# Performance work log

Measured on AMD Instinct MI355X. Metric: run time of the kernel, lower is better.

The kernel has to match this reference:

```python
import jax, jax.numpy as jnp
import numpy as np

EMBED_DIM = 1024
NUM_HEADS = 16
HEAD_DIM = EMBED_DIM // NUM_HEADS
BATCH, SEQ = 1, 4096


def setup_inputs() -> dict:
    key = jax.random.key(0)
    k1, k2, k3 = jax.random.split(key, 3)
    hidden_states = jax.random.normal(k1, (BATCH, SEQ, EMBED_DIM), dtype=jnp.float32)
    W_qkv = jax.random.normal(k2, (3 * EMBED_DIM, EMBED_DIM), dtype=jnp.float32) * 0.02
    b_qkv = jnp.zeros((3 * EMBED_DIM,), dtype=jnp.float32)
    # torch init: identity per head, perturb slightly to make test non-trivial
    eye = jnp.broadcast_to(jnp.eye(HEAD_DIM, dtype=jnp.float32), (NUM_HEADS, HEAD_DIM, HEAD_DIM))
    hebbian_trace = eye + 0.01 * jax.random.normal(k3, (NUM_HEADS, HEAD_DIM, HEAD_DIM), dtype=jnp.float32)
    return {"hidden_states": hidden_states, "W_qkv": W_qkv, "b_qkv": b_qkv, "hebbian_trace": hebbian_trace}


def reference(hidden_states, W_qkv, b_qkv, hebbian_trace):
    B, S, E = hidden_states.shape
    H, D = NUM_HEADS, HEAD_DIM
    qkv = hidden_states @ W_qkv.T + b_qkv              # [B,S,3E]
    q, k, v = jnp.split(qkv, 3, axis=-1)
    # [B,H,S,D]
    q = q.reshape(B, S, H, D).transpose(0, 2, 1, 3)
    k = k.reshape(B, S, H, D).transpose(0, 2, 1, 3)
    v = v.reshape(B, S, H, D).transpose(0, 2, 1, 3)
    scores = jnp.einsum('bhqd,bhkd->bhqk', q, k) / jnp.sqrt(jnp.float32(D))
    attn = jax.nn.softmax(scores, axis=-1)
    weighted_v = jnp.einsum('bhqk,bhkd->bhqd', attn, v)  # [B,H,S,D]
    # torch einsum 'blhd,hdd->blhd': repeated 'd' in trace -> diagonal scaling
    wv = weighted_v.transpose(0, 2, 1, 3)               # [B,S,H,D]
    v_transformed = jnp.einsum('blhd,hdd->blhd', wv, hebbian_trace)
    return v_transformed.reshape(B, S, E)
```

## Files before the change

### kernel.cpp

```cpp
#include <hip/hip_runtime.h>
#include <hip/hip_bf16.h>
#include <stdint.h>

#define S_LEN 4096

typedef short s16x8  __attribute__((ext_vector_type(8)));
typedef float f32x4  __attribute__((ext_vector_type(4)));
typedef float f32x16 __attribute__((ext_vector_type(16)));

#define CEXP 0.18033688011112042f

__device__ __forceinline__ unsigned short f2bf(float f) {
    union { float f; unsigned u; } v; v.f = f;
    unsigned r = v.u + 0x7fffu + ((v.u >> 16) & 1u);
    return (unsigned short)(r >> 16);
}

__device__ __forceinline__ ushort2 pkbf(float a, float b) {
    float2 f; f.x = a; f.y = b;
    __hip_bfloat162 h = __float22bfloat162_rn(f);
    union { __hip_bfloat162 h; ushort2 u; } cv; cv.h = h;
    return cv.u;
}

__device__ __forceinline__ ushort4 pkbf4(float x, float y, float z, float w) {
    ushort2 lo = pkbf(x, y), hi = pkbf(z, w);
    ushort4 r; r.x = lo.x; r.y = lo.y; r.z = hi.x; r.w = hi.y;
    return r;
}

typedef const __attribute__((address_space(1))) void* gas_t;
typedef __attribute__((address_space(3))) void* sas_t;

__device__ __forceinline__ void async16(const void* g, void* s) {
    __builtin_amdgcn_global_load_lds((gas_t)g, (sas_t)s, 16, 0, 0);
}

__global__ __launch_bounds__(256) void cvt_bf16(
    const float* __restrict__ X, const float* __restrict__ W,
    unsigned short* __restrict__ Xb, unsigned short* __restrict__ Wb)
{
    const long NX = 4194304;
    long i = (long)(blockIdx.x * 256 + threadIdx.x) * 8;
    const float* src; unsigned short* dst; long off;
    if (i < NX) { src = X; dst = Xb; off = i; }
    else        { src = W; dst = Wb; off = i - NX; }
    float4 a = *(const float4*)(src + off);
    float4 b = *(const float4*)(src + off + 4);
    union { s16x8 v; ushort4 q[2]; } o;
    o.q[0] = pkbf4(a.x, a.y, a.z, a.w);
    o.q[1] = pkbf4(b.x, b.y, b.z, b.w);
    *(s16x8*)(dst + off) = o.v;
}

__global__ __launch_bounds__(256) void qkv_gemm_bf16(
    const unsigned short* __restrict__ Xb, const unsigned short* __restrict__ Wb,
    const float* __restrict__ bias, const float* __restrict__ trace,
    unsigned short* __restrict__ Qb, unsigned short* __restrict__ Kb,
    unsigned short* __restrict__ Vt)
{
    __shared__ __align__(16) unsigned short sm[17408];
    unsigned short* As = sm;
    unsigned short* Bs = sm + 8192;

    const int t = threadIdx.x;
    const int l = t & 63;
    const int w = t >> 6;
    const int bid = blockIdx.x;
    const int xcd = bid & 7;
    const int ii  = bid >> 3;
    const int bn  = 3 * xcd + (ii % 3);
    const int bm  = ii / 3;
    const int rowBase = (w >> 1) * 64;
    const int colBase = (w & 1) * 64;

    f32x4 acc[4][4];
#pragma unroll
    for (int i = 0; i < 4; i++)
#pragma unroll
        for (int j = 0; j < 4; j++) acc[i][j] = (f32x4)0.f;

    const int srow = l >> 3;
    const int scol = (l & 7) * 8;

    for (int kt = 0; kt < 16; ++kt) {
        const int k0 = kt * 64;
#pragma unroll
        for (int c = 0; c < 4; ++c) {
            int m = w * 4 + c;
            const unsigned short* ga = Xb + (bm * 128 + m * 8 + srow) * 1024 + k0 + scol;
            const unsigned short* gb = Wb + (bn * 128 + m * 8 + srow) * 1024 + k0 + scol;
            async16(ga, As + m * 512);
            async16(gb, Bs + m * 512);
        }
        __syncthreads();

#pragma unroll
        for (int kc = 0; kc < 2; ++kc) {
            s16x8 af[4], bf[4];
#pragma unroll
            for (int i = 0; i < 4; i++) {
                af[i] = *(const s16x8*)(As + (rowBase + i * 16 + (l & 15)) * 64 + kc * 32 + (l >> 4) * 8);
                bf[i] = *(const s16x8*)(Bs + (colBase + i * 16 + (l & 15)) * 64 + kc * 32 + (l >> 4) * 8);
            }
#pragma unroll
            for (int i = 0; i < 4; i++)
#pragma unroll
                for (int j = 0; j < 4; j++)
                    acc[i][j] = __builtin_amdgcn_mfma_f32_16x16x32_bf16(af[i], bf[j], acc[i][j], 0, 0, 0);
        }
        __syncthreads();
    }

    if (bn < 16) {
        __syncthreads();
        unsigned short* Lt = sm;
        const int region = bn >> 3;
        const float scl = (region == 0) ? CEXP : 1.0f;
#pragma unroll
        for (int j = 0; j < 4; j++) {
            int cl = colBase + j * 16 + (l & 15);
            float bv = bias[bn * 128 + cl];
#pragma unroll
            for (int i = 0; i < 4; i++) {
                int s0 = rowBase + i * 16 + ((l >> 4) << 2);
#pragma unroll
                for (int r = 0; r < 4; r++)
                    Lt[(s0 + r) * 136 + cl] = f2bf((acc[i][j][r] + bv) * scl);
            }
        }
        __syncthreads();
        unsigned short* dst = (region == 0) ? Qb : Kb;
        const int h0 = (bn & 7) * 2;
#pragma unroll
        for (int p = 0; p < 8; ++p) {
            int linear = p * 256 + t;
            int sl = linear >> 4;
            int ch = linear & 15;
            int d  = (ch & 7) * 8;
            int h  = h0 + (ch >> 3);
            s16x8 v = *(const s16x8*)(Lt + sl * 136 + ch * 8);
            *(s16x8*)(dst + (h * S_LEN + bm * 128 + sl) * 64 + d) = v;
        }
    } else {
        __syncthreads();
        unsigned short* Lt = sm;
#pragma unroll
        for (int j = 0; j < 4; j++) {
            int cl = colBase + j * 16 + (l & 15);
            int o  = bn * 128 + cl - 2048;
            float bv = bias[bn * 128 + cl];
            float tr = trace[(o >> 6) * 4096 + (o & 63) * 65];
#pragma unroll
            for (int i = 0; i < 4; i++) {
                int s0 = rowBase + i * 16 + ((l >> 4) << 2);
                *(ushort4*)(Lt + cl * 136 + s0) =
                    pkbf4((acc[i][j][0] + bv) * tr, (acc[i][j][1] + bv) * tr,
                          (acc[i][j][2] + bv) * tr, (acc[i][j][3] + bv) * tr);
            }
        }
        __syncthreads();
#pragma unroll
        for (int p = 0; p < 8; ++p) {
            int dl  = (t >> 4) + p * 16;
            int sch = (t & 15) * 8;
            int o = bn * 128 + dl - 2048;
            int h = o >> 6, d = o & 63;
            s16x8 v = *(const s16x8*)(Lt + dl * 136 + sch);
            *(s16x8*)(Vt + (h * 64 + d) * S_LEN + bm * 128 + sch) = v;
        }
    }
}

__global__ __launch_bounds__(256) void qkv_gemm_f32(
    const float* __restrict__ X, const float* __restrict__ W,
    const float* __restrict__ bias, const float* __restrict__ trace,
    unsigned short* __restrict__ Qb, unsigned short* __restrict__ Kb,
    unsigned short* __restrict__ Vt)
{
    __shared__ __align__(16) unsigned short sm[17408];
    unsigned short* As = sm;
    unsigned short* Bs = sm + 5120;

    const int t = threadIdx.x;
    const int l = t & 63;
    const int w = t >> 6;
    const int bm = blockIdx.y, bn = blockIdx.x;
    const int rowBase = (w >> 1) * 64;
    const int colBase = (w & 1) * 64;

    f32x4 acc[4][4];
#pragma unroll
    for (int i = 0; i < 4; i++)
#pragma unroll
        for (int j = 0; j < 4; j++) acc[i][j] = (f32x4)0.f;

    const int sr = t >> 3;
    const int sc = (t & 7) * 4;

    for (int kt = 0; kt < 32; ++kt) {
        const int k0 = kt * 32;
#pragma unroll
        for (int p = 0; p < 4; ++p) {
            int r = sr + p * 32;
            float4 xa = *(const float4*)(X + (bm * 128 + r) * 1024 + k0 + sc);
            float4 wb = *(const float4*)(W + (bn * 128 + r) * 1024 + k0 + sc);
            *(ushort4*)(As + r * 40 + sc) = pkbf4(xa.x, xa.y, xa.z, xa.w);
            *(ushort4*)(Bs + r * 40 + sc) = pkbf4(wb.x, wb.y, wb.z, wb.w);
        }
        __syncthreads();

        s16x8 af[4], bf[4];
#pragma unroll
        for (int i = 0; i < 4; i++) {
            af[i] = *(const s16x8*)(As + (rowBase + i * 16 + (l & 15)) * 40 + (l >> 4) * 8);
            bf[i] = *(const s16x8*)(Bs + (colBase + i * 16 + (l & 15)) * 40 + (l >> 4) * 8);
        }
#pragma unroll
        for (int i = 0; i < 4; i++)
#pragma unroll
            for (int j = 0; j < 4; j++)
                acc[i][j] = __builtin_amdgcn_mfma_f32_16x16x32_bf16(af[i], bf[j], acc[i][j], 0, 0, 0);
        __syncthreads();
    }

    if (bn < 16) {
        __syncthreads();
        unsigned short* Lt = sm;
        const int region = bn >> 3;
        const float scl = (region == 0) ? CEXP : 1.0f;
#pragma unroll
        for (int j = 0; j < 4; j++) {
            int cl = colBase + j * 16 + (l & 15);
            float bv = bias[bn * 128 + cl];
#pragma unroll
            for (int i = 0; i < 4; i++) {
                int s0 = rowBase + i * 16 + ((l >> 4) << 2);
#pragma unroll
                for (int r = 0; r < 4; r++)
                    Lt[(s0 + r) * 136 + cl] = f2bf((acc[i][j][r] + bv) * scl);
            }
        }
        __syncthreads();
        unsigned short* dst = (region == 0) ? Qb : Kb;
        const int h0 = (bn & 7) * 2;
#pragma unroll
        for (int p = 0; p < 8; ++p) {
            int linear = p * 256 + t;
            int sl = linear >> 4;
            int ch = linear & 15;
            int d  = (ch & 7) * 8;
            int h  = h0 + (ch >> 3);
            s16x8 v = *(const s16x8*)(Lt + sl * 136 + ch * 8);
            *(s16x8*)(dst + (h * S_LEN + bm * 128 + sl) * 64 + d) = v;
        }
    } else {
        __syncthreads();
        unsigned short* Lt = sm;
#pragma unroll
        for (int j = 0; j < 4; j++) {
            int cl = colBase + j * 16 + (l & 15);
            int o  = bn * 128 + cl - 2048;
            float bv = bias[bn * 128 + cl];
            float tr = trace[(o >> 6) * 4096 + (o & 63) * 65];
#pragma unroll
            for (int i = 0; i < 4; i++) {
                int s0 = rowBase + i * 16 + ((l >> 4) << 2);
                *(ushort4*)(Lt + cl * 136 + s0) =
                    pkbf4((acc[i][j][0] + bv) * tr, (acc[i][j][1] + bv) * tr,
                          (acc[i][j][2] + bv) * tr, (acc[i][j][3] + bv) * tr);
            }
        }
        __syncthreads();
#pragma unroll
        for (int p = 0; p < 8; ++p) {
            int dl  = (t >> 4) + p * 16;
            int sch = (t & 15) * 8;
            int o = bn * 128 + dl - 2048;
            int h = o >> 6, d = o & 63;
            s16x8 v = *(const s16x8*)(Lt + dl * 136 + sch);
            *(s16x8*)(Vt + (h * 64 + d) * S_LEN + bm * 128 + sch) = v;
        }
    }
}

__global__ __launch_bounds__(512, 4) void attn(
    const unsigned short* __restrict__ Qb, const unsigned short* __restrict__ Kb,
    const unsigned short* __restrict__ Vt, float* __restrict__ out)
{
    __shared__ __align__(16) unsigned short sm[35840];
    __shared__ float lArr[256];

    const int t = threadIdx.x;
    const int l = t & 63;
    const int w = t >> 6;
    const int g = w >> 2;
    const int wq = w & 3;
    const int h = blockIdx.y;
    const int qbase = blockIdx.x * 128 + wq * 32;
    const int l31 = l & 31;
    const int lh  = l >> 5;

    unsigned short* Ks  = sm + g * 9216;
    unsigned short* Vts = sm + g * 9216 + 4608;
    unsigned short* Pw  = sm + 18432 + w * 2176 + l31 * 68;

    s16x8 qf[4];
#pragma unroll
    for (int ks = 0; ks < 4; ks++)
        qf[ks] = *(const s16x8*)(Qb + (h * S_LEN + qbase + l31) * 64 + ks * 16 + lh * 8);

    f32x16 O0 = (f32x16)0.f, O1 = (f32x16)0.f;
    float2 lpA; lpA.x = 0.f; lpA.y = 0.f;
    float2 lpB; lpB.x = 0.f; lpB.y = 0.f;

    const int tg    = t & 255;
    const int strow = tg >> 2;
    const int stch  = (tg & 3) * 16;

    const unsigned short* kbase = Kb + (h * S_LEN + strow) * 64 + stch;
    const unsigned short* vbase = Vt + (h * 64 + strow) * S_LEN + stch;

    s16x8 k0v, k1v, v0v, v1v;
    {
        const int kv0 = g * 2048;
        k0v = *(const s16x8*)(kbase + kv0 * 64);
        k1v = *(const s16x8*)(kbase + kv0 * 64 + 8);
        v0v = *(const s16x8*)(vbase + kv0);
        v1v = *(const s16x8*)(vbase + kv0 + 8);
    }

    for (int kt = 0; kt < 32; ++kt) {
        *(s16x8*)(Ks  + strow * 72 + stch)     = k0v;
        *(s16x8*)(Ks  + strow * 72 + stch + 8) = k1v;
        *(s16x8*)(Vts + strow * 72 + stch)     = v0v;
        *(s16x8*)(Vts + strow * 72 + stch + 8) = v1v;
        __syncthreads();

        {
            const int kvn = g * 2048 + ((kt + 1) & 31) * 64;
            k0v = *(const s16x8*)(kbase + kvn * 64);
            k1v = *(const s16x8*)(kbase + kvn * 64 + 8);
            v0v = *(const s16x8*)(vbase + kvn);
            v1v = *(const s16x8*)(vbase + kvn + 8);
        }

        f32x16 S0 = (f32x16)0.f, S1 = (f32x16)0.f;
#pragma unroll
        for (int ks = 0; ks < 4; ks++) {
            s16x8 a0 = *(const s16x8*)(Ks + l31 * 72 + ks * 16 + lh * 8);
            s16x8 a1 = *(const s16x8*)(Ks + (32 + l31) * 72 + ks * 16 + lh * 8);
            S0 = __builtin_amdgcn_mfma_f32_32x32x16_bf16(a0, qf[ks], S0, 0, 0, 0);
            S1 = __builtin_amdgcn_mfma_f32_32x32x16_bf16(a1, qf[ks], S1, 0, 0, 0);
        }

#pragma unroll
        for (int i = 0; i < 16; i += 4) {
            float p0 = __builtin_amdgcn_exp2f(S0[i+0]); S0[i+0] = p0; lpA.x += p0;
            float p1 = __builtin_amdgcn_exp2f(S0[i+1]); S0[i+1] = p1; lpA.y += p1;
            float p2 = __builtin_amdgcn_exp2f(S0[i+2]); S0[i+2] = p2; lpB.x += p2;
            float p3 = __builtin_amdgcn_exp2f(S0[i+3]); S0[i+3] = p3; lpB.y += p3;
        }
#pragma unroll
        for (int i = 0; i < 16; i += 4) {
            float p0 = __builtin_amdgcn_exp2f(S1[i+0]); S1[i+0] = p0; lpA.x += p0;
            float p1 = __builtin_amdgcn_exp2f(S1[i+1]); S1[i+1] = p1; lpA.y += p1;
            float p2 = __builtin_amdgcn_exp2f(S1[i+2]); S1[i+2] = p2; lpB.x += p2;
            float p3 = __builtin_amdgcn_exp2f(S1[i+3]); S1[i+3] = p3; lpB.y += p3;
        }

#pragma unroll
        for (int gq = 0; gq < 4; ++gq) {
            *(ushort4*)(Pw + gq * 8 + lh * 4)      = pkbf4(S0[gq*4], S0[gq*4+1], S0[gq*4+2], S0[gq*4+3]);
            *(ushort4*)(Pw + 32 + gq * 8 + lh * 4) = pkbf4(S1[gq*4], S1[gq*4+1], S1[gq*4+2], S1[gq*4+3]);
        }

#pragma unroll
        for (int ks = 0; ks < 4; ks++) {
            union { s16x8 v; ushort4 q[2]; } pu;
            pu.q[0] = *(const ushort4*)(Pw + ks * 16 + lh * 8);
            pu.q[1] = *(const ushort4*)(Pw + ks * 16 + lh * 8 + 4);
            s16x8 av0 = *(const s16x8*)(Vts + l31 * 72 + ks * 16 + lh * 8);
            s16x8 av1 = *(const s16x8*)(Vts + (32 + l31) * 72 + ks * 16 + lh * 8);
            O0 = __builtin_amdgcn_mfma_f32_32x32x16_bf16(av0, pu.v, O0, 0, 0, 0);
            O1 = __builtin_amdgcn_mfma_f32_32x32x16_bf16(av1, pu.v, O1, 0, 0, 0);
        }
        __syncthreads();
    }

    float l_part = (lpA.x + lpA.y) + (lpB.x + lpB.y);
    float l_tot = l_part + __shfl_xor(l_part, 32);
    if (lh == 0) lArr[w * 32 + l31] = l_tot;

    float* Lo = (float*)sm + w * 2176;
#pragma unroll
    for (int dt = 0; dt < 2; ++dt) {
        const f32x16& Ox = dt ? O1 : O0;
#pragma unroll
        for (int gq = 0; gq < 4; ++gq) {
            int d0 = dt * 32 + gq * 8 + lh * 4;
            float4 vv;
            vv.x = Ox[gq*4+0]; vv.y = Ox[gq*4+1]; vv.z = Ox[gq*4+2]; vv.w = Ox[gq*4+3];
            *(float4*)(Lo + l31 * 68 + d0) = vv;
        }
    }
    __syncthreads();

    if (w < 4) {
        const float* LoA = (float*)sm + w * 2176;
        const float* LoB = (float*)sm + (w + 4) * 2176;
#pragma unroll
        for (int it = 0; it < 8; ++it) {
            int ql = it * 4 + (l >> 4);
            float invl = 1.0f / (lArr[w * 32 + ql] + lArr[(w + 4) * 32 + ql]);
            float4 a = *(const float4*)(LoA + ql * 68 + (l & 15) * 4);
            float4 b = *(const float4*)(LoB + ql * 68 + (l & 15) * 4);
            float4 vv;
            vv.x = (a.x + b.x) * invl;
            vv.y = (a.y + b.y) * invl;
            vv.z = (a.z + b.z) * invl;
            vv.w = (a.w + b.w) * invl;
            *(float4*)(out + (blockIdx.x * 128 + w * 32 + ql) * 1024 + h * 64 + (l & 15) * 4) = vv;
        }
    }
}

extern "C" void kernel_launch(void* const* d_in, const int* in_sizes, int n_in,
                              void* d_out, int out_size, void* d_ws, size_t ws_size,
                              hipStream_t stream) {
    const float* X     = (const float*)d_in[0];
    const float* W     = (const float*)d_in[1];
    const float* bias  = (const float*)d_in[2];
    const float* trace = (const float*)d_in[3];
    float* out = (float*)d_out;

    unsigned short* Qb = (unsigned short*)d_ws;
    unsigned short* Kb = Qb + 4194304;
    unsigned short* Vt = Kb + 4194304;
    unsigned short* Xb = Vt + 4194304;
    unsigned short* Wb = Xb + 4194304;

    const size_t NEED_BF16 = (size_t)3 * 8388608 + 8388608 + 6291456;

    if (ws_size >= NEED_BF16) {
        cvt_bf16<<<3584, 256, 0, stream>>>(X, W, Xb, Wb);
        qkv_gemm_bf16<<<768, 256, 0, stream>>>(Xb, Wb, bias, trace, Qb, Kb, Vt);
    } else {
        qkv_gemm_f32<<<dim3(24, 32), 256, 0, stream>>>(X, W, bias, trace, Qb, Kb, Vt);
    }
    attn<<<dim3(32, 16), 512, 0, stream>>>(Qb, Kb, Vt, out);
}
```

Measured before the change: 218.1 us.

## Load K/V fragments directly from global into registers, drop shared staging and barriers

After: 358.9 us. 64.6% more time.

```diff
diff --git a/kernel.cpp b/kernel.cpp
--- a/kernel.cpp
+++ b/kernel.cpp
@@ -288,8 +288,9 @@
     const unsigned short* __restrict__ Qb, const unsigned short* __restrict__ Kb,
     const unsigned short* __restrict__ Vt, float* __restrict__ out)
 {
-    __shared__ __align__(16) unsigned short sm[35840];
-    __shared__ float lArr[256];
+    __shared__ __align__(16) float Lo[4][2176];
+    __shared__ __align__(16) unsigned short Ps[8][640];
+    __shared__ float lArr[128];
 
     const int t = threadIdx.x;
     const int l = t & 63;
@@ -301,57 +302,37 @@
     const int l31 = l & 31;
     const int lh  = l >> 5;
 
-    unsigned short* Ks  = sm + g * 9216;
-    unsigned short* Vts = sm + g * 9216 + 4608;
-    unsigned short* Pw  = sm + 18432 + w * 2176 + l31 * 68;
+    unsigned short* Pc = Ps[w];
 
     s16x8 qf[4];
 #pragma unroll
     for (int ks = 0; ks < 4; ks++)
         qf[ks] = *(const s16x8*)(Qb + (h * S_LEN + qbase + l31) * 64 + ks * 16 + lh * 8);
+
+    const unsigned short* kp0 = Kb + (h * S_LEN + g * 2048 + l31) * 64 + lh * 8;
+    const unsigned short* kp1 = kp0 + 32 * 64;
+    const unsigned short* vp0 = Vt + (h * 64 + l31) * S_LEN + g * 2048 + lh * 8;
+    const unsigned short* vp1 = vp0 + 32 * S_LEN;
 
     f32x16 O0 = (f32x16)0.f, O1 = (f32x16)0.f;
     float2 lpA; lpA.x = 0.f; lpA.y = 0.f;
     float2 lpB; lpB.x = 0.f; lpB.y = 0.f;
 
-    const int tg    = t & 255;
-    const int strow = tg >> 2;
-    const int stch  = (tg & 3) * 16;
-
-    const unsigned short* kbase = Kb + (h * S_LEN + strow) * 64 + stch;
-    const unsigned short* vbase = Vt + (h * 64 + strow) * S_LEN + stch;
-
-    s16x8 k0v, k1v, v0v, v1v;
-    {
-        const int kv0 = g * 2048;
-        k0v = *(const s16x8*)(kbase + kv0 * 64);
-        k1v = *(const s16x8*)(kbase + kv0 * 64 + 8);
-        v0v = *(const s16x8*)(vbase + kv0);
-        v1v = *(const s16x8*)(vbase + kv0 + 8);
-    }
-
     for (int kt = 0; kt < 32; ++kt) {
-        *(s16x8*)(Ks  + strow * 72 + stch)     = k0v;
-        *(s16x8*)(Ks  + strow * 72 + stch + 8) = k1v;
-        *(s16x8*)(Vts + strow * 72 + stch)     = v0v;
-        *(s16x8*)(Vts + strow * 72 + stch + 8) = v1v;
-        __syncthreads();
-
-        {
-            const int kvn = g * 2048 + ((kt + 1) & 31) * 64;
-            k0v = *(const s16x8*)(kbase + kvn * 64);
-            k1v = *(const s16x8*)(kbase + kvn * 64 + 8);
-            v0v = *(const s16x8*)(vbase + kvn);
-            v1v = *(const s16x8*)(vbase + kvn + 8);
-        }
-
+        const int koff = kt * 4096;
+        const int voff = kt * 64;
+
+        s16x8 ka0[4], ka1[4];
+#pragma unroll
+        for (int ks = 0; ks < 4; ++ks) {
+            ka0[ks] = *(const s16x8*)(kp0 + koff + ks * 16);
+            ka1[ks] = *(const s16x8*)(kp1 + koff + ks * 16);
+        }
         f32x16 S0 = (f32x16)0.f, S1 = (f32x16)0.f;
 #pragma unroll
-        for (int ks = 0; ks < 4; ks++) {
-            s16x8 a0 = *(const s16x8*)(Ks + l31 * 72 + ks * 16 + lh * 8);
-            s16x8 a1 = *(const s16x8*)(Ks + (32 + l31) * 72 + ks * 16 + lh * 8);
-            S0 = __builtin_amdgcn_mfma_f32_32x32x16_bf16(a0, qf[ks], S0, 0, 0, 0);
-            S1 = __builtin_amdgcn_mfma_f32_32x32x16_bf16(a1, qf[ks], S1, 0, 0, 0);
+        for (int ks = 0; ks < 4; ++ks) {
+            S0 = __builtin_amdgcn_mfma_f32_32x32x16_bf16(ka0[ks], qf[ks], S0, 0, 0, 0);
+            S1 = __builtin_amdgcn_mfma_f32_32x32x16_bf16(ka1[ks], qf[ks], S1, 0, 0, 0);
         }
 
 #pragma unroll
@@ -370,58 +351,81 @@
         }
 
 #pragma unroll
-        for (int gq = 0; gq < 4; ++gq) {
-            *(ushort4*)(Pw + gq * 8 + lh * 4)      = pkbf4(S0[gq*4], S0[gq*4+1], S0[gq*4+2], S0[gq*4+3]);
-            *(ushort4*)(Pw + 32 + gq * 8 + lh * 4) = pkbf4(S1[gq*4], S1[gq*4+1], S1[gq*4+2], S1[gq*4+3]);
-        }
-
-#pragma unroll
-        for (int ks = 0; ks < 4; ks++) {
+        for (int ks = 0; ks < 4; ++ks) {
+            ushort4 qL, qH;
+            if (ks == 0) {
+                qL = pkbf4(S0[0], S0[1], S0[2], S0[3]);
+                qH = pkbf4(S0[4], S0[5], S0[6], S0[7]);
+            } else if (ks == 1) {
+                qL = pkbf4(S0[8], S0[9], S0[10], S0[11]);
+                qH = pkbf4(S0[12], S0[13], S0[14], S0[15]);
+            } else if (ks == 2) {
+                qL = pkbf4(S1[0], S1[1], S1[2], S1[3]);
+                qH = pkbf4(S1[4], S1[5], S1[6], S1[7]);
+            } else {
+                qL = pkbf4(S1[8], S1[9], S1[10], S1[11]);
+                qH = pkbf4(S1[12], S1[13], S1[14], S1[15]);
+            }
+            *(ushort4*)(Pc + l31 * 20 + 4 * lh)     = qL;
+            *(ushort4*)(Pc + l31 * 20 + 8 + 4 * lh) = qH;
+
             union { s16x8 v; ushort4 q[2]; } pu;
-            pu.q[0] = *(const ushort4*)(Pw + ks * 16 + lh * 8);
-            pu.q[1] = *(const ushort4*)(Pw + ks * 16 + lh * 8 + 4);
-            s16x8 av0 = *(const s16x8*)(Vts + l31 * 72 + ks * 16 + lh * 8);
-            s16x8 av1 = *(const s16x8*)(Vts + (32 + l31) * 72 + ks * 16 + lh * 8);
+            pu.q[0] = *(const ushort4*)(Pc + l31 * 20 + lh * 8);
+            pu.q[1] = *(const ushort4*)(Pc + l31 * 20 + lh * 8 + 4);
+
+            s16x8 av0 = *(const s16x8*)(vp0 + voff + ks * 16);
+            s16x8 av1 = *(const s16x8*)(vp1 + voff + ks * 16);
             O0 = __builtin_amdgcn_mfma_f32_32x32x16_bf16(av0, pu.v, O0, 0, 0, 0);
             O1 = __builtin_amdgcn_mfma_f32_32x32x16_bf16(av1, pu.v, O1, 0, 0, 0);
         }
-        __syncthreads();
     }
 
     float l_part = (lpA.x + lpA.y) + (lpB.x + lpB.y);
     float l_tot = l_part + __shfl_xor(l_part, 32);
-    if (lh == 0) lArr[w * 32 + l31] = l_tot;
-
-    float* Lo = (float*)sm + w * 2176;
-#pragma unroll
-    for (int dt = 0; dt < 2; ++dt) {
-        const f32x16& Ox = dt ? O1 : O0;
-#pragma unroll
-        for (int gq = 0; gq < 4; ++gq) {
-            int d0 = dt * 32 + gq * 8 + lh * 4;
-            float4 vv;
-            vv.x = Ox[gq*4+0]; vv.y = Ox[gq*4+1]; vv.z = Ox[gq*4+2]; vv.w = Ox[gq*4+3];
-            *(float4*)(Lo + l31 * 68 + d0) = vv;
-        }
-    }
+
     __syncthreads();
-
+    if (w >= 4) {
+        if (lh == 0) lArr[(w - 4) * 32 + l31] = l_tot;
+        float* Ls = Lo[w - 4];
+#pragma unroll
+        for (int dt = 0; dt < 2; ++dt) {
+            const f32x16& Ox = dt ? O1 : O0;
+#pragma unroll
+            for (int gq = 0; gq < 4; ++gq) {
+                int d0 = dt * 32 + gq * 8 + lh * 4;
+                float4 vv;
+                vv.x = Ox[gq*4+0]; vv.y = Ox[gq*4+1]; vv.z = Ox[gq*4+2]; vv.w = Ox[gq*4+3];
+                *(float4*)(Ls + l31 * 68 + d0) = vv;
+            }
+        }
+    }
+    __syncthreads();
     if (w < 4) {
-        const float* LoA = (float*)sm + w * 2176;
-        const float* LoB = (float*)sm + (w + 4) * 2176;
-#pragma unroll
-        for (int it = 0; it < 8; ++it) {
-            int ql = it * 4 + (l >> 4);
-            float invl = 1.0f / (lArr[w * 32 + ql] + lArr[(w + 4) * 32 + ql]);
-            float4 a = *(const float4*)(LoA + ql * 68 + (l & 15) * 4);
-            float4 b = *(const float4*)(LoB + ql * 68 + (l & 15) * 4);
-            float4 vv;
-            vv.x = (a.x + b.x) * invl;
-            vv.y = (a.y + b.y) * invl;
-            vv.z = (a.z + b.z) * invl;
-            vv.w = (a.w + b.w) * invl;
-            *(float4*)(out + (blockIdx.x * 128 + w * 32 + ql) * 1024 + h * 64 + (l & 15) * 4) = vv;
-        }
+        float invl = 1.0f / (l_tot + lArr[w * 32 + l31]);
+        float* Ls = Lo[w];
+#pragma unroll
+        for (int dt = 0; dt < 2; ++dt) {
+            const f32x16& Ox = dt ? O1 : O0;
+#pragma unroll
+            for (int gq = 0; gq < 4; ++gq) {
+                int d0 = dt * 32 + gq * 8 + lh * 4;
+                float4 p = *(const float4*)(Ls + l31 * 68 + d0);
+                p.x = (p.x + Ox[gq*4+0]) * invl;
+                p.y = (p.y + Ox[gq*4+1]) * invl;
+                p.z = (p.z + Ox[gq*4+2]) * invl;
+                p.w = (p.w + Ox[gq*4+3]) * invl;
+                *(float4*)(Ls + l31 * 68 + d0) = p;
+            }
+        }
+    }
+    __syncthreads();
+#pragma unroll
+    for (int it = 0; it < 4; ++it) {
+        int linear = it * 512 + t;
+        int row = linear >> 4;
+        int c   = (linear & 15) * 4;
+        float4 v = *(const float4*)(Lo[row >> 5] + (row & 31) * 68 + c);
+        *(float4*)(out + (blockIdx.x * 128 + row) * 1024 + h * 64 + c) = v;
     }
 }
 
```

## Split attention over KV halves with combine kernel and XCD-aware head mapping

Applied to the files above, without the earlier changes.

Result: slower. 224.7 us (+3.0%).

```diff
diff --git a/kernel.cpp b/kernel.cpp
--- a/kernel.cpp
+++ b/kernel.cpp
@@ -66,11 +66,7 @@
     const int t = threadIdx.x;
     const int l = t & 63;
     const int w = t >> 6;
-    const int bid = blockIdx.x;
-    const int xcd = bid & 7;
-    const int ii  = bid >> 3;
-    const int bn  = 3 * xcd + (ii % 3);
-    const int bm  = ii / 3;
+    const int bm = blockIdx.y, bn = blockIdx.x;
     const int rowBase = (w >> 1) * 64;
     const int colBase = (w & 1) * 64;
 
@@ -284,7 +280,184 @@
     }
 }
 
-__global__ __launch_bounds__(512, 4) void attn(
+__global__ __launch_bounds__(512, 4) void attn_split(
+    const unsigned short* __restrict__ Qb, const unsigned short* __restrict__ Kb,
+    const unsigned short* __restrict__ Vt,
+    float* __restrict__ wsO, float* __restrict__ wsL)
+{
+    __shared__ __align__(16) unsigned short sm[18432];
+    __shared__ float lArr[128];
+
+    const int t = threadIdx.x;
+    const int l = t & 63;
+    const int w = t >> 6;
+    const int g = w >> 2;
+    const int wq = w & 3;
+    const int bid = blockIdx.x;
+    const int xcd = bid & 7;
+    const int j   = bid >> 3;
+    const int h   = xcd * 2 + (j & 1);
+    const int kvh = (j >> 1) & 1;
+    const int qblk = j >> 2;
+    const int qbase = qblk * 128 + wq * 32;
+    const int l31 = l & 31;
+    const int lh  = l >> 5;
+
+    unsigned short* Ks  = sm + g * 9216;
+    unsigned short* Vts = sm + g * 9216 + 4608;
+
+    s16x8 qf[4];
+#pragma unroll
+    for (int ks = 0; ks < 4; ks++)
+        qf[ks] = *(const s16x8*)(Qb + (h * S_LEN + qbase + l31) * 64 + ks * 16 + lh * 8);
+
+    f32x16 O0 = (f32x16)0.f, O1 = (f32x16)0.f;
+    float2 lpA; lpA.x = 0.f; lpA.y = 0.f;
+    float2 lpB; lpB.x = 0.f; lpB.y = 0.f;
+
+    const int tg    = t & 255;
+    const int strow = tg >> 2;
+    const int stch  = (tg & 3) * 16;
+    const int kv00  = kvh * 2048 + g * 1024;
+
+    for (int kt = 0; kt < 16; ++kt) {
+        const int kv0 = kv00 + kt * 64;
+        {
+            const unsigned short* ksrc = Kb + (h * S_LEN + kv0 + strow) * 64 + stch;
+            const unsigned short* vsrc = Vt + (h * 64 + strow) * S_LEN + kv0 + stch;
+            s16x8 k0v = *(const s16x8*)(ksrc);
+            s16x8 k1v = *(const s16x8*)(ksrc + 8);
+            s16x8 v0v = *(const s16x8*)(vsrc);
+            s16x8 v1v = *(const s16x8*)(vsrc + 8);
+            *(s16x8*)(Ks  + strow * 72 + stch)     = k0v;
+            *(s16x8*)(Ks  + strow * 72 + stch + 8) = k1v;
+            *(s16x8*)(Vts + strow * 72 + stch)     = v0v;
+            *(s16x8*)(Vts + strow * 72 + stch + 8) = v1v;
+        }
+        __syncthreads();
+
+        f32x16 S0 = (f32x16)0.f, S1 = (f32x16)0.f;
+#pragma unroll
+        for (int ks = 0; ks < 4; ks++) {
+            s16x8 a0 = *(const s16x8*)(Ks + l31 * 72 + ks * 16 + lh * 8);
+            s16x8 a1 = *(const s16x8*)(Ks + (32 + l31) * 72 + ks * 16 + lh * 8);
+            S0 = __builtin_amdgcn_mfma_f32_32x32x16_bf16(a0, qf[ks], S0, 0, 0, 0);
+            S1 = __builtin_amdgcn_mfma_f32_32x32x16_bf16(a1, qf[ks], S1, 0, 0, 0);
+        }
+
+#pragma unroll
+        for (int i = 0; i < 16; i += 4) {
+            float p0 = __builtin_amdgcn_exp2f(S0[i+0]); S0[i+0] = p0; lpA.x += p0;
+            float p1 = __builtin_amdgcn_exp2f(S0[i+1]); S0[i+1] = p1; lpA.y += p1;
+            float p2 = __builtin_amdgcn_exp2f(S0[i+2]); S0[i+2] = p2; lpB.x += p2;
+            float p3 = __builtin_amdgcn_exp2f(S0[i+3]); S0[i+3] = p3; lpB.y += p3;
+        }
+#pragma unroll
+        for (int i = 0; i < 16; i += 4) {
+            float p0 = __builtin_amdgcn_exp2f(S1[i+0]); S1[i+0] = p0; lpA.x += p0;
+            float p1 = __builtin_amdgcn_exp2f(S1[i+1]); S1[i+1] = p1; lpA.y += p1;
+            float p2 = __builtin_amdgcn_exp2f(S1[i+2]); S1[i+2] = p2; lpB.x += p2;
+            float p3 = __builtin_amdgcn_exp2f(S1[i+3]); S1[i+3] = p3; lpB.y += p3;
+        }
+
+#pragma unroll
+        for (int ks = 0; ks < 4; ks++) {
+            const f32x16& S = (ks < 2) ? S0 : S1;
+            const int qa = (ks & 1) * 8;
+            ushort4 pA = pkbf4(S[qa+0], S[qa+1], S[qa+2], S[qa+3]);
+            ushort4 pB = pkbf4(S[qa+4], S[qa+5], S[qa+6], S[qa+7]);
+            union { ushort4 q; uint2 u; } cA, cB; cA.q = pA; cB.q = pB;
+            uint2 send; send.x = lh ? cA.u.x : cB.u.x; send.y = lh ? cA.u.y : cB.u.y;
+            uint2 recv;
+            recv.x = (unsigned)__shfl_xor((int)send.x, 32);
+            recv.y = (unsigned)__shfl_xor((int)send.y, 32);
+            union { s16x8 v; uint2 u2[2]; } pf;
+            pf.u2[0].x = lh ? recv.x : cA.u.x;
+            pf.u2[0].y = lh ? recv.y : cA.u.y;
+            pf.u2[1].x = lh ? cB.u.x : recv.x;
+            pf.u2[1].y = lh ? cB.u.y : recv.y;
+
+            s16x8 av0 = *(const s16x8*)(Vts + l31 * 72 + ks * 16 + lh * 8);
+            s16x8 av1 = *(const s16x8*)(Vts + (32 + l31) * 72 + ks * 16 + lh * 8);
+            O0 = __builtin_amdgcn_mfma_f32_32x32x16_bf16(av0, pf.v, O0, 0, 0, 0);
+            O1 = __builtin_amdgcn_mfma_f32_32x32x16_bf16(av1, pf.v, O1, 0, 0, 0);
+        }
+        __syncthreads();
+    }
+
+    float l_part = (lpA.x + lpA.y) + (lpB.x + lpB.y);
+    float l_tot = l_part + __shfl_xor(l_part, 32);
+
+    float* Lo = (float*)sm;
+    if (g == 1) {
+        if (lh == 0) lArr[wq * 32 + l31] = l_tot;
+        float* Ls = Lo + wq * 2176;
+#pragma unroll
+        for (int dt = 0; dt < 2; ++dt) {
+            const f32x16& Ox = dt ? O1 : O0;
+#pragma unroll
+            for (int gq = 0; gq < 4; ++gq) {
+                int d0 = dt * 32 + gq * 8 + lh * 4;
+                float4 vv;
+                vv.x = Ox[gq*4+0]; vv.y = Ox[gq*4+1]; vv.z = Ox[gq*4+2]; vv.w = Ox[gq*4+3];
+                *(float4*)(Ls + l31 * 68 + d0) = vv;
+            }
+        }
+    }
+    __syncthreads();
+    if (g == 0) {
+        float lsum = l_tot + lArr[wq * 32 + l31];
+        if (lh == 0) wsL[kvh * 65536 + h * 4096 + qbase + l31] = lsum;
+        float* Ls = Lo + wq * 2176;
+#pragma unroll
+        for (int dt = 0; dt < 2; ++dt) {
+            const f32x16& Ox = dt ? O1 : O0;
+#pragma unroll
+            for (int gq = 0; gq < 4; ++gq) {
+                int d0 = dt * 32 + gq * 8 + lh * 4;
+                float4 p = *(const float4*)(Ls + l31 * 68 + d0);
+                p.x += Ox[gq*4+0]; p.y += Ox[gq*4+1];
+                p.z += Ox[gq*4+2]; p.w += Ox[gq*4+3];
+                *(float4*)(Ls + l31 * 68 + d0) = p;
+            }
+        }
+    }
+    __syncthreads();
+#pragma unroll
+    for (int it = 0; it < 4; ++it) {
+        int linear = it * 512 + t;
+        int row = linear >> 4;
+        int c   = (linear & 15) * 4;
+        float4 v = *(const float4*)(Lo + (row >> 5) * 2176 + (row & 31) * 68 + c);
+        *(float4*)(wsO + (((size_t)(kvh * 16 + h) * 4096) + qblk * 128 + row) * 64 + c) = v;
+    }
+}
+
+__global__ __launch_bounds__(256) void attn_combine(
+    const float* __restrict__ wsO, const float* __restrict__ wsL,
+    float* __restrict__ out)
+{
+    int gidx = blockIdx.x * 256 + threadIdx.x;
+    int base = gidx * 4;
+    int s = base >> 10;
+    int e = base & 1023;
+    int h = e >> 6, d0 = e & 63;
+    float la = wsL[h * 4096 + s];
+    float lb = wsL[65536 + h * 4096 + s];
+    float inv = 1.0f / (la + lb);
+    const float* pa = wsO + ((size_t)h * 4096 + s) * 64 + d0;
+    const float* pb = wsO + ((size_t)(16 + h) * 4096 + s) * 64 + d0;
+    float4 a = *(const float4*)pa;
+    float4 b = *(const float4*)pb;
+    float4 v;
+    v.x = (a.x + b.x) * inv;
+    v.y = (a.y + b.y) * inv;
+    v.z = (a.z + b.z) * inv;
+    v.w = (a.w + b.w) * inv;
+    *(float4*)(out + base) = v;
+}
+
+__global__ __launch_bounds__(512, 4) void attn_full(
     const unsigned short* __restrict__ Qb, const unsigned short* __restrict__ Kb,
     const unsigned short* __restrict__ Vt, float* __restrict__ out)
 {
@@ -296,8 +469,12 @@
     const int w = t >> 6;
     const int g = w >> 2;
     const int wq = w & 3;
-    const int h = blockIdx.y;
-    const int qbase = blockIdx.x * 128 + wq * 32;
+    const int bid = blockIdx.x;
+    const int xcd = bid & 7;
+    const int j   = bid >> 3;
+    const int h   = xcd * 2 + (j & 1);
+    const int qblk = j >> 1;
+    const int qbase = qblk * 128 + wq * 32;
     const int l31 = l & 31;
     const int lh  = l >> 5;
 
@@ -318,32 +495,21 @@
     const int strow = tg >> 2;
     const int stch  = (tg & 3) * 16;
 
-    const unsigned short* kbase = Kb + (h * S_LEN + strow) * 64 + stch;
-    const unsigned short* vbase = Vt + (h * 64 + strow) * S_LEN + stch;
-
-    s16x8 k0v, k1v, v0v, v1v;
-    {
-        const int kv0 = g * 2048;
-        k0v = *(const s16x8*)(kbase + kv0 * 64);
-        k1v = *(const s16x8*)(kbase + kv0 * 64 + 8);
-        v0v = *(const s16x8*)(vbase + kv0);
-        v1v = *(const s16x8*)(vbase + kv0 + 8);
-    }
-
     for (int kt = 0; kt < 32; ++kt) {
-        *(s16x8*)(Ks  + strow * 72 + stch)     = k0v;
-        *(s16x8*)(Ks  + strow * 72 + stch + 8) = k1v;
-        *(s16x8*)(Vts + strow * 72 + stch)     = v0v;
-        *(s16x8*)(Vts + strow * 72 + stch + 8) = v1v;
-        __syncthreads();
-
+        const int kv0 = g * 2048 + kt * 64;
         {
-            const int kvn = g * 2048 + ((kt + 1) & 31) * 64;
-            k0v = *(const s16x8*)(kbase + kvn * 64);
-            k1v = *(const s16x8*)(kbase + kvn * 64 + 8);
-            v0v = *(const s16x8*)(vbase + kvn);
-            v1v = *(const s16x8*)(vbase + kvn + 8);
-        }
+            const unsigned short* ksrc = Kb + (h * S_LEN + kv0 + strow) * 64 + stch;
+            const unsigned short* vsrc = Vt + (h * 64 + strow) * S_LEN + kv0 + stch;
+            s16x8 k0v = *(const s16x8*)(ksrc);
+            s16x8 k1v = *(const s16x8*)(ksrc + 8);
+            s16x8 v0v = *(const s16x8*)(vsrc);
+            s16x8 v1v = *(const s16x8*)(vsrc + 8);
+            *(s16x8*)(Ks  + strow * 72 + stch)     = k0v;
+            *(s16x8*)(Ks  + strow * 72 + stch + 8) = k1v;
+            *(s16x8*)(Vts + strow * 72 + stch)     = v0v;
+            *(s16x8*)(Vts + strow * 72 + stch + 8) = v1v;
+        }
+        __syncthreads();
 
         f32x16 S0 = (f32x16)0.f, S1 = (f32x16)0.f;
 #pragma unroll
@@ -420,7 +586,7 @@
             vv.y = (a.y + b.y) * invl;
             vv.z = (a.z + b.z) * invl;
             vv.w = (a.w + b.w) * invl;
-            *(float4*)(out + (blockIdx.x * 128 + w * 32 + ql) * 1024 + h * 64 + (l & 15) * 4) = vv;
+            *(float4*)(out + (qblk * 128 + w * 32 + ql) * 1024 + h * 64 + (l & 15) * 4) = vv;
         }
     }
 }
@@ -439,14 +605,23 @@
     unsigned short* Vt = Kb + 4194304;
     unsigned short* Xb = Vt + 4194304;
     unsigned short* Wb = Xb + 4194304;
-
-    const size_t NEED_BF16 = (size_t)3 * 8388608 + 8388608 + 6291456;
-
-    if (ws_size >= NEED_BF16) {
+    float* wsO = (float*)Xb;
+    float* wsL = (float*)((char*)d_ws + 58720256);
+
+    const size_t NEED_SPLIT = 58720256 + 524288;
+    const size_t NEED_BF16  = (size_t)3 * 8388608 + 8388608 + 6291456;
+
+    if (ws_size >= NEED_SPLIT) {
         cvt_bf16<<<3584, 256, 0, stream>>>(X, W, Xb, Wb);
-        qkv_gemm_bf16<<<768, 256, 0, stream>>>(Xb, Wb, bias, trace, Qb, Kb, Vt);
+        qkv_gemm_bf16<<<dim3(24, 32), 256, 0, stream>>>(Xb, Wb, bias, trace, Qb, Kb, Vt);
+        attn_split<<<1024, 512, 0, stream>>>(Qb, Kb, Vt, wsO, wsL);
+        attn_combine<<<4096, 256, 0, stream>>>(wsO, wsL, out);
+    } else if (ws_size >= NEED_BF16) {
+        cvt_bf16<<<3584, 256, 0, stream>>>(X, W, Xb, Wb);
+        qkv_gemm_bf16<<<dim3(24, 32), 256, 0, stream>>>(Xb, Wb, bias, trace, Qb, Kb, Vt);
+        attn_full<<<512, 512, 0, stream>>>(Qb, Kb, Vt, out);
     } else {
         qkv_gemm_f32<<<dim3(24, 32), 256, 0, stream>>>(X, W, bias, trace, Qb, Kb, Vt);
-    }
-    attn<<<dim3(32, 16), 512, 0, stream>>>(Qb, Kb, Vt, out);
-}
+        attn_full<<<512, 512, 0, stream>>>(Qb, Kb, Vt, out);
+    }
+}
```
